# Kernel tuning notes

Measured on AMD Instinct MI355X. Metric: run time of the kernel, lower is better.

## Reference

```python
import jax, jax.numpy as jnp
import numpy as np


def setup_inputs() -> dict:
    key = jax.random.key(0)
    # x: [B, C, T, M] = [64, 4, 8192, 16]
    x = jax.random.normal(key, (64, 4, 8192, 16), dtype=jnp.float32)
    return {"x": x}


def reference(x) -> jnp.ndarray:
    # torch.cov(row[c].T): variables = last dim M, observations = T, correction=1.
    # Output: [B, C, M, M]
    T = x.shape[2]
    xc = x - jnp.mean(x, axis=2, keepdims=True)        # center over time axis
    cov = jnp.einsum('bctm,bctn->bcmn', xc, xc) / (T - 1)
    return cov
```

## Files before the change

### kernel.cpp

```cpp
#include <hip/hip_runtime.h>


constexpr int T_DIM = 8192;
constexpr int M_DIM = 16;
constexpr int BLOCK = 1024;
constexpr int NWAVE = BLOCK / 64;
constexpr int T_PER_WAVE = T_DIM / NWAVE;
constexpr int ROUNDS = T_PER_WAVE / 32;
constexpr int PF = 4;

using bf16x8 = __attribute__((ext_vector_type(8))) short;
using f32x4  = __attribute__((ext_vector_type(4))) float;

static __device__ inline unsigned pack_bf2(float lo, float hi) {
    union { float f; unsigned u; } a{lo}, b{hi};
    unsigned ra = a.u + 0x7fffu + ((a.u >> 16) & 1u);
    unsigned rb = b.u + 0x7fffu + ((b.u >> 16) & 1u);
    return (ra >> 16) | (rb & 0xffff0000u);
}

__global__ __launch_bounds__(BLOCK)
void cov_kernel(const float* __restrict__ x, float* __restrict__ out) {
    const int bc   = blockIdx.x;
    const int tid  = threadIdx.x;
    const int wave = tid >> 6;
    const int lane = tid & 63;

    const int rg = lane >> 2;
    const int g  = lane & 3;
    const int q  = lane >> 4;
    const int m  = lane & 15;

    __shared__ __align__(16) unsigned stage[NWAVE][2][256];
    __shared__ float Pred[NWAVE][256];
    __shared__ float Sred[NWAVE][M_DIM];
    __shared__ float Stot[M_DIM];

    const f32x4* __restrict__ xin =
        (const f32x4*)(x + (size_t)bc * (T_DIM * M_DIM));

    const int idx0 = wave * (T_PER_WAVE * 4) + lane;

    const int qw = rg >> 2, dq = rg & 3;
    const int roff = (q * 16 + (m ^ q)) * 4;

    f32x4 acc = {0.f, 0.f, 0.f, 0.f};
    float s0 = 0.f, s1 = 0.f, s2 = 0.f, s3 = 0.f;

    f32x4 buf0[PF], buf1[PF];
#pragma unroll
    for (int r = 0; r < PF; ++r) {
        buf0[r] = __builtin_nontemporal_load(&xin[idx0 + r * 128]);
        buf1[r] = __builtin_nontemporal_load(&xin[idx0 + r * 128 + 64]);
    }

#pragma unroll
    for (int r = 0; r < ROUNDS; ++r) {
        const f32x4 a0 = buf0[r % PF];
        const f32x4 a1 = buf1[r % PF];
        if (r + PF < ROUNDS) {
            buf0[r % PF] =
                __builtin_nontemporal_load(&xin[idx0 + (r + PF) * 128]);
            buf1[r % PF] =
                __builtin_nontemporal_load(&xin[idx0 + (r + PF) * 128 + 64]);
        }

        s0 += a0[0] + a1[0];  s1 += a0[1] + a1[1];
        s2 += a0[2] + a1[2];  s3 += a0[3] + a1[3];
        unsigned* wb = &stage[wave][r & 1][0];
        wb[(qw * 16 + ((4 * g + 0) ^ qw)) * 4 + dq] = pack_bf2(a0[0], a1[0]);
        wb[(qw * 16 + ((4 * g + 1) ^ qw)) * 4 + dq] = pack_bf2(a0[1], a1[1]);
        wb[(qw * 16 + ((4 * g + 2) ^ qw)) * 4 + dq] = pack_bf2(a0[2], a1[2]);
        wb[(qw * 16 + ((4 * g + 3) ^ qw)) * 4 + dq] = pack_bf2(a0[3], a1[3]);
        bf16x8 frag = *(const bf16x8*)&stage[wave][r & 1][roff];
        acc = __builtin_amdgcn_mfma_f32_16x16x32_bf16(frag, frag, acc, 0, 0, 0);
    }

#pragma unroll
    for (int off = 4; off <= 32; off <<= 1) {
        s0 += __shfl_xor(s0, off, 64);
        s1 += __shfl_xor(s1, off, 64);
        s2 += __shfl_xor(s2, off, 64);
        s3 += __shfl_xor(s3, off, 64);
    }
    if (rg == 0) {
        Sred[wave][4 * g + 0] = s0;
        Sred[wave][4 * g + 1] = s1;
        Sred[wave][4 * g + 2] = s2;
        Sred[wave][4 * g + 3] = s3;
    }

#pragma unroll
    for (int r = 0; r < 4; ++r)
        Pred[wave][(q * 4 + r) * M_DIM + m] = acc[r];
    __syncthreads();

    if (tid < M_DIM) {
        float s = 0.f;
#pragma unroll
        for (int w = 0; w < NWAVE; ++w) s += Sred[w][tid];
        Stot[tid] = s;
    }
    __syncthreads();

    if (tid < 256) {
        float P = 0.f;
#pragma unroll
        for (int w = 0; w < NWAVE; ++w) P += Pred[w][tid];
        const int mi = tid >> 4;
        const int ni = tid & 15;
        const float cov = (P - Stot[mi] * Stot[ni] * (1.0f / (float)T_DIM))
                        * (1.0f / (float)(T_DIM - 1));
        out[(size_t)bc * 256 + tid] = cov;
    }
}

extern "C" void kernel_launch(void* const* d_in, const int* in_sizes, int n_in,
                              void* d_out, int out_size, void* d_ws, size_t ws_size,
                              hipStream_t stream) {
    const float* x = (const float*)d_in[0];
    float* out = (float*)d_out;
    const int n_bc = in_sizes[0] / (T_DIM * M_DIM);
    cov_kernel<<<dim3(n_bc), dim3(BLOCK), 0, stream>>>(x, out);
}
```

Before: 177.8 us.

## Replace bf16 MFMA Gram accumulation with fp32 FMAs using DPP quad exchange

Drops the LDS-staged bf16 packing and MFMA path. Each thread now loads one float4 per round and builds the 16x16 outer-product sum in fp32 FMAs, using DPP quad permutes to fetch the other three column groups from neighbouring lanes. The block shrinks to 512 threads with a min-blocks hint of 2, and the nontemporal loads become plain loads. This removes LDS traffic and barriers in the main loop and the bf16 rounding error, at the cost of 64 accumulator registers per thread, more VALU work and a larger cross-lane reduction at the end.

Result: slower. 194.5 us (+9.4%).

```diff
diff --git a/kernel.cpp b/kernel.cpp
--- a/kernel.cpp
+++ b/kernel.cpp
@@ -1,116 +1,142 @@
 #include <hip/hip_runtime.h>
 
 
-constexpr int T_DIM = 8192;
-constexpr int M_DIM = 16;
-constexpr int BLOCK = 1024;
-constexpr int NWAVE = BLOCK / 64;
-constexpr int T_PER_WAVE = T_DIM / NWAVE;
-constexpr int ROUNDS = T_PER_WAVE / 32;
-constexpr int PF = 4;
+constexpr int T_DIM  = 8192;
+constexpr int M_DIM  = 16;
+constexpr int BLOCK  = 512;
+constexpr int NWAVE  = BLOCK / 64;
+constexpr int ROUNDS = T_DIM * M_DIM / 4 / BLOCK;
+constexpr int PF     = 4;
 
-using bf16x8 = __attribute__((ext_vector_type(8))) short;
-using f32x4  = __attribute__((ext_vector_type(4))) float;
+using f32x4 = __attribute__((ext_vector_type(4))) float;
 
-static __device__ inline unsigned pack_bf2(float lo, float hi) {
-    union { float f; unsigned u; } a{lo}, b{hi};
-    unsigned ra = a.u + 0x7fffu + ((a.u >> 16) & 1u);
-    unsigned rb = b.u + 0x7fffu + ((b.u >> 16) & 1u);
-    return (ra >> 16) | (rb & 0xffff0000u);
+template <int CTRL>
+static __device__ inline float qperm(float x) {
+    int xi = __builtin_bit_cast(int, x);
+    int r  = __builtin_amdgcn_update_dpp(xi, xi, CTRL, 0xF, 0xF, true);
+    return __builtin_bit_cast(float, r);
 }
+constexpr int DPP_XOR1 = 0xB1;
+constexpr int DPP_XOR2 = 0x4E;
+constexpr int DPP_XOR3 = 0x1B;
 
-__global__ __launch_bounds__(BLOCK)
+__global__ __launch_bounds__(BLOCK, 2)
 void cov_kernel(const float* __restrict__ x, float* __restrict__ out) {
     const int bc   = blockIdx.x;
     const int tid  = threadIdx.x;
     const int wave = tid >> 6;
     const int lane = tid & 63;
+    const int qt   = lane & 3;
 
-    const int rg = lane >> 2;
-    const int g  = lane & 3;
-    const int q  = lane >> 4;
-    const int m  = lane & 15;
-
-    __shared__ __align__(16) unsigned stage[NWAVE][2][256];
-    __shared__ float Pred[NWAVE][256];
-    __shared__ float Sred[NWAVE][M_DIM];
+    __shared__ float Pred[NWAVE * 4 * 64];
+    __shared__ float Sred[NWAVE * 4 * 4];
     __shared__ float Stot[M_DIM];
 
     const f32x4* __restrict__ xin =
         (const f32x4*)(x + (size_t)bc * (T_DIM * M_DIM));
 
-    const int idx0 = wave * (T_PER_WAVE * 4) + lane;
+    float acc[4][4][4];
+#pragma unroll
+    for (int i = 0; i < 4; ++i)
+#pragma unroll
+        for (int d = 0; d < 4; ++d)
+#pragma unroll
+            for (int j = 0; j < 4; ++j) acc[i][d][j] = 0.f;
+    float s[4] = {0.f, 0.f, 0.f, 0.f};
 
-    const int qw = rg >> 2, dq = rg & 3;
-    const int roff = (q * 16 + (m ^ q)) * 4;
+    auto do_round = [&](const f32x4 v) {
+        float c1[4], c2[4], c3[4];
+#pragma unroll
+        for (int j = 0; j < 4; ++j) {
+            c1[j] = qperm<DPP_XOR1>(v[j]);
+            c2[j] = qperm<DPP_XOR2>(v[j]);
+            c3[j] = qperm<DPP_XOR3>(v[j]);
+        }
+#pragma unroll
+        for (int i = 0; i < 4; ++i) {
+            s[i] += v[i];
+#pragma unroll
+            for (int j = 0; j < 4; ++j) {
+                acc[i][0][j] = fmaf(v[i], v[j],  acc[i][0][j]);
+                acc[i][1][j] = fmaf(v[i], c1[j], acc[i][1][j]);
+                acc[i][2][j] = fmaf(v[i], c2[j], acc[i][2][j]);
+                acc[i][3][j] = fmaf(v[i], c3[j], acc[i][3][j]);
+            }
+        }
+    };
 
-    f32x4 acc = {0.f, 0.f, 0.f, 0.f};
-    float s0 = 0.f, s1 = 0.f, s2 = 0.f, s3 = 0.f;
+    f32x4 buf[PF];
+#pragma unroll
+    for (int r = 0; r < PF; ++r) buf[r] = xin[(size_t)r * BLOCK + tid];
 
-    f32x4 buf0[PF], buf1[PF];
+    for (int it = 0; it < ROUNDS / PF - 1; ++it) {
 #pragma unroll
-    for (int r = 0; r < PF; ++r) {
-        buf0[r] = __builtin_nontemporal_load(&xin[idx0 + r * 128]);
-        buf1[r] = __builtin_nontemporal_load(&xin[idx0 + r * 128 + 64]);
+        for (int u = 0; u < PF; ++u) {
+            const f32x4 v = buf[u];
+            buf[u] = xin[(size_t)((it + 1) * PF + u) * BLOCK + tid];
+            do_round(v);
+        }
     }
+#pragma unroll
+    for (int u = 0; u < PF; ++u) do_round(buf[u]);
 
 #pragma unroll
-    for (int r = 0; r < ROUNDS; ++r) {
-        const f32x4 a0 = buf0[r % PF];
-        const f32x4 a1 = buf1[r % PF];
-        if (r + PF < ROUNDS) {
-            buf0[r % PF] =
-                __builtin_nontemporal_load(&xin[idx0 + (r + PF) * 128]);
-            buf1[r % PF] =
-                __builtin_nontemporal_load(&xin[idx0 + (r + PF) * 128 + 64]);
+    for (int i = 0; i < 4; ++i)
+#pragma unroll
+        for (int d = 0; d < 4; ++d)
+#pragma unroll
+            for (int j = 0; j < 4; ++j) {
+                float a = acc[i][d][j];
+                a += __shfl_xor(a, 4, 64);
+                a += __shfl_xor(a, 8, 64);
+                a += __shfl_xor(a, 16, 64);
+                a += __shfl_xor(a, 32, 64);
+                acc[i][d][j] = a;
+            }
+#pragma unroll
+    for (int i = 0; i < 4; ++i) {
+        float a = s[i];
+        a += __shfl_xor(a, 4, 64);
+        a += __shfl_xor(a, 8, 64);
+        a += __shfl_xor(a, 16, 64);
+        a += __shfl_xor(a, 32, 64);
+        s[i] = a;
+    }
+    if (lane < 4) {
+#pragma unroll
+        for (int i = 0; i < 4; ++i) {
+#pragma unroll
+            for (int d = 0; d < 4; ++d)
+#pragma unroll
+                for (int j = 0; j < 4; ++j)
+                    Pred[(wave * 4 + qt) * 64 + (i * 16 + d * 4 + j)] =
+                        acc[i][d][j];
+            Sred[(wave * 4 + qt) * 4 + i] = s[i];
         }
-
-        s0 += a0[0] + a1[0];  s1 += a0[1] + a1[1];
-        s2 += a0[2] + a1[2];  s3 += a0[3] + a1[3];
-        unsigned* wb = &stage[wave][r & 1][0];
-        wb[(qw * 16 + ((4 * g + 0) ^ qw)) * 4 + dq] = pack_bf2(a0[0], a1[0]);
-        wb[(qw * 16 + ((4 * g + 1) ^ qw)) * 4 + dq] = pack_bf2(a0[1], a1[1]);
-        wb[(qw * 16 + ((4 * g + 2) ^ qw)) * 4 + dq] = pack_bf2(a0[2], a1[2]);
-        wb[(qw * 16 + ((4 * g + 3) ^ qw)) * 4 + dq] = pack_bf2(a0[3], a1[3]);
-        bf16x8 frag = *(const bf16x8*)&stage[wave][r & 1][roff];
-        acc = __builtin_amdgcn_mfma_f32_16x16x32_bf16(frag, frag, acc, 0, 0, 0);
     }
-
-#pragma unroll
-    for (int off = 4; off <= 32; off <<= 1) {
-        s0 += __shfl_xor(s0, off, 64);
-        s1 += __shfl_xor(s1, off, 64);
-        s2 += __shfl_xor(s2, off, 64);
-        s3 += __shfl_xor(s3, off, 64);
-    }
-    if (rg == 0) {
-        Sred[wave][4 * g + 0] = s0;
-        Sred[wave][4 * g + 1] = s1;
-        Sred[wave][4 * g + 2] = s2;
-        Sred[wave][4 * g + 3] = s3;
-    }
-
-#pragma unroll
-    for (int r = 0; r < 4; ++r)
-        Pred[wave][(q * 4 + r) * M_DIM + m] = acc[r];
     __syncthreads();
 
     if (tid < M_DIM) {
-        float s = 0.f;
+        const int a_ = tid >> 2, i = tid & 3;
+        float ssum = 0.f;
 #pragma unroll
-        for (int w = 0; w < NWAVE; ++w) s += Sred[w][tid];
-        Stot[tid] = s;
+        for (int w = 0; w < NWAVE; ++w) ssum += Sred[(w * 4 + a_) * 4 + i];
+        Stot[tid] = ssum;
     }
     __syncthreads();
 
     if (tid < 256) {
+        const int m = tid >> 4, n = tid & 15;
+        const int a_ = m >> 2, i = m & 3;
+        const int b_ = n >> 2, j = n & 3;
+        const int d  = a_ ^ b_;
+        const int p  = i * 16 + d * 4 + j;
         float P = 0.f;
 #pragma unroll
-        for (int w = 0; w < NWAVE; ++w) P += Pred[w][tid];
-        const int mi = tid >> 4;
-        const int ni = tid & 15;
-        const float cov = (P - Stot[mi] * Stot[ni] * (1.0f / (float)T_DIM))
-                        * (1.0f / (float)(T_DIM - 1));
+        for (int w = 0; w < NWAVE; ++w) P += Pred[(w * 4 + a_) * 64 + p];
+        const float cov =
+            (P - Stot[m] * Stot[n] * (1.0f / (float)T_DIM)) *
+            (1.0f / (float)(T_DIM - 1));
         out[(size_t)bc * 256 + tid] = cov;
     }
 }
```

## Split covariance over time segments into partial and final reduction kernels

Applied to the files above, without the earlier changes.

Replaces the one-block-per-(b,c) 1024-thread kernel with a two-kernel split-T scheme. Each (b,c) is divided into 8 time segments handled by 256-thread blocks that write partial Gram matrices and column sums to workspace. A second kernel sums the partials and applies the mean correction. This raises the block count from 256 to 2048 to fill all CUs and hide memory latency better, at the cost of a second launch and some workspace traffic.

After: 177.8 us. No clear change (-0.0%).

```diff
diff --git a/kernel.cpp b/kernel.cpp
--- a/kernel.cpp
+++ b/kernel.cpp
@@ -3,11 +3,14 @@
 
 constexpr int T_DIM = 8192;
 constexpr int M_DIM = 16;
-constexpr int BLOCK = 1024;
-constexpr int NWAVE = BLOCK / 64;
-constexpr int T_PER_WAVE = T_DIM / NWAVE;
+constexpr int NSEG  = 8;
+constexpr int T_SEG = T_DIM / NSEG;
+constexpr int BLOCK1 = 256;
+constexpr int NWAVE1 = BLOCK1 / 64;
+constexpr int T_PER_WAVE = T_SEG / NWAVE1;
 constexpr int ROUNDS = T_PER_WAVE / 32;
 constexpr int PF = 4;
+constexpr int WS_STRIDE = 272;
 
 using bf16x8 = __attribute__((ext_vector_type(8))) short;
 using f32x4  = __attribute__((ext_vector_type(4))) float;
@@ -19,9 +22,11 @@
     return (ra >> 16) | (rb & 0xffff0000u);
 }
 
-__global__ __launch_bounds__(BLOCK)
-void cov_kernel(const float* __restrict__ x, float* __restrict__ out) {
-    const int bc   = blockIdx.x;
+__global__ __launch_bounds__(BLOCK1, 8)
+void cov_partial(const float* __restrict__ x, float* __restrict__ ws) {
+    const int blk  = blockIdx.x;
+    const int bc   = blk >> 3;
+    const int seg  = blk & (NSEG - 1);
     const int tid  = threadIdx.x;
     const int wave = tid >> 6;
     const int lane = tid & 63;
@@ -31,13 +36,12 @@
     const int q  = lane >> 4;
     const int m  = lane & 15;
 
-    __shared__ __align__(16) unsigned stage[NWAVE][2][256];
-    __shared__ float Pred[NWAVE][256];
-    __shared__ float Sred[NWAVE][M_DIM];
-    __shared__ float Stot[M_DIM];
+    __shared__ __align__(16) unsigned stage[NWAVE1][2][256];
+    __shared__ float Pred[NWAVE1][256];
+    __shared__ float Sred[NWAVE1][M_DIM];
 
     const f32x4* __restrict__ xin =
-        (const f32x4*)(x + (size_t)bc * (T_DIM * M_DIM));
+        (const f32x4*)(x + ((size_t)bc * T_DIM + (size_t)seg * T_SEG) * M_DIM);
 
     const int idx0 = wave * (T_PER_WAVE * 4) + lane;
 
@@ -95,24 +99,45 @@
         Pred[wave][(q * 4 + r) * M_DIM + m] = acc[r];
     __syncthreads();
 
+    {
+        float P = 0.f;
+#pragma unroll
+        for (int w = 0; w < NWAVE1; ++w) P += Pred[w][tid];
+        ws[(size_t)blk * WS_STRIDE + tid] = P;
+    }
     if (tid < M_DIM) {
         float s = 0.f;
 #pragma unroll
-        for (int w = 0; w < NWAVE; ++w) s += Sred[w][tid];
+        for (int w = 0; w < NWAVE1; ++w) s += Sred[w][tid];
+        ws[(size_t)blk * WS_STRIDE + 256 + tid] = s;
+    }
+}
+
+__global__ __launch_bounds__(256)
+void cov_final(const float* __restrict__ ws, float* __restrict__ out) {
+    const int bc  = blockIdx.x;
+    const int tid = threadIdx.x;
+    __shared__ float Stot[M_DIM];
+
+    if (tid < M_DIM) {
+        float s = 0.f;
+#pragma unroll
+        for (int q = 0; q < NSEG; ++q)
+            s += ws[((size_t)bc * NSEG + q) * WS_STRIDE + 256 + tid];
         Stot[tid] = s;
     }
     __syncthreads();
 
-    if (tid < 256) {
-        float P = 0.f;
+    float P = 0.f;
 #pragma unroll
-        for (int w = 0; w < NWAVE; ++w) P += Pred[w][tid];
-        const int mi = tid >> 4;
-        const int ni = tid & 15;
-        const float cov = (P - Stot[mi] * Stot[ni] * (1.0f / (float)T_DIM))
-                        * (1.0f / (float)(T_DIM - 1));
-        out[(size_t)bc * 256 + tid] = cov;
-    }
+    for (int q = 0; q < NSEG; ++q)
+        P += ws[((size_t)bc * NSEG + q) * WS_STRIDE + tid];
+
+    const int mi = tid >> 4;
+    const int ni = tid & 15;
+    const float cov = (P - Stot[mi] * Stot[ni] * (1.0f / (float)T_DIM))
+                    * (1.0f / (float)(T_DIM - 1));
+    out[(size_t)bc * 256 + tid] = cov;
 }
 
 extern "C" void kernel_launch(void* const* d_in, const int* in_sizes, int n_in,
@@ -120,6 +145,8 @@
                               hipStream_t stream) {
     const float* x = (const float*)d_in[0];
     float* out = (float*)d_out;
+    float* ws  = (float*)d_ws;
     const int n_bc = in_sizes[0] / (T_DIM * M_DIM);
-    cov_kernel<<<dim3(n_bc), dim3(BLOCK), 0, stream>>>(x, out);
+    cov_partial<<<dim3(n_bc * NSEG), dim3(BLOCK1), 0, stream>>>(x, ws);
+    cov_final<<<dim3(n_bc), dim3(256), 0, stream>>>(ws, out);
 }
```
